# Performance work log

Hardware: AMD Instinct MI355X
Metric: run time of the kernel (lower is better)

The kernel has to match this reference:

```python
import jax, jax.numpy as jnp
import numpy as np

WS = 7
SHIFT = 3
NH = 16
DIM = 512
MLP = 2048
EMB = 512
EPS = 1e-6


def _rel_pos_index(ws):
    coords = np.stack(np.meshgrid(np.arange(ws), np.arange(ws), indexing='ij'))  # [2,ws,ws]
    flat = coords.reshape(2, -1)
    rel = flat[:, :, None] - flat[:, None, :]          # [2,N,N]
    rel = rel.transpose(1, 2, 0).copy()                # [N,N,2]
    rel[..., 0] += ws - 1
    rel[..., 1] += ws - 1
    rel[..., 0] *= 2 * ws - 1
    return rel.sum(-1)                                 # [N,N] int


def _shift_mask(H, W, ws, shift):
    img = np.zeros((H, W))
    cnt = 0
    for hs in (slice(0, -ws), slice(-ws, -shift), slice(-shift, None)):
        for wsl in (slice(0, -ws), slice(-ws, -shift), slice(-shift, None)):
            img[hs, wsl] = cnt
            cnt += 1
    win = img.reshape(H // ws, ws, W // ws, ws).transpose(0, 2, 1, 3).reshape(-1, ws * ws)
    diff = win[:, None, :] - win[:, :, None]           # [nW,N,N]
    return np.where(diff != 0, -100.0, 0.0).astype(np.float32)


def setup_inputs() -> dict:
    key = jax.random.key(0)
    ks = jax.random.split(key, 16)
    B, H, W = 16, 56, 56
    C, mlp, emb_dim = DIM, MLP, EMB
    std = 0.02
    inp = {
        'x': jax.random.normal(ks[0], (B, H * W, C), jnp.float32),
        'emb': jax.random.normal(ks[1], (B, emb_dim), jnp.float32),
        'adaLN_w': jax.random.normal(ks[2], (emb_dim, 6 * C), jnp.float32) * std,
        'adaLN_b': jnp.zeros((6 * C,), jnp.float32),
        'qkv_w': jax.random.normal(ks[3], (C, 3 * C), jnp.float32) * std,
        'qkv_b': jnp.zeros((3 * C,), jnp.float32),
        'proj_w': jax.random.normal(ks[4], (C, C), jnp.float32) * std,
        'proj_b': jnp.zeros((C,), jnp.float32),
        'rel_bias_table': jax.random.normal(ks[5], ((2 * WS - 1) ** 2, NH), jnp.float32) * std,
        'ff_w1': jax.random.normal(ks[6], (C, mlp), jnp.float32) * std,
        'ff_b1': jnp.zeros((mlp,), jnp.float32),
        'ff_w2': jax.random.normal(ks[7], (mlp, C), jnp.float32) * std,
        'ff_b2': jnp.zeros((C,), jnp.float32),
        'H': H,
        'W': W,
    }
    return inp


def _ln(t):
    mu = t.mean(-1, keepdims=True)
    var = ((t - mu) ** 2).mean(-1, keepdims=True)
    return (t - mu) / jnp.sqrt(var + EPS)


def reference(x, emb, adaLN_w, adaLN_b, qkv_w, qkv_b, proj_w, proj_b,
              rel_bias_table, ff_w1, ff_b1, ff_w2, ff_b2, H, W):
    B, L, C = x.shape
    dh = C // NH
    scale = dh ** (-0.5)
    N = WS * WS
    nWh, nWw = H // WS, W // WS
    nW = nWh * nWw

    # AdaLN modulation
    mod = jax.nn.silu(emb) @ adaLN_w + adaLN_b
    sh_sa, sc_sa, g_sa, sh_ff, sc_ff, g_ff = jnp.split(mod, 6, axis=-1)

    h = _ln(x) * (1.0 + sc_sa[:, None, :]) + sh_sa[:, None, :]
    h = h.reshape(B, H, W, C)
    h = jnp.roll(h, (-SHIFT, -SHIFT), axis=(1, 2))

    # window partition -> [B*nW, N, C]
    win = h.reshape(B, nWh, WS, nWw, WS, C).transpose(0, 1, 3, 2, 4, 5).reshape(B * nW, N, C)

    qkv = (win @ qkv_w + qkv_b).reshape(B * nW, N, 3, NH, dh).transpose(2, 0, 3, 1, 4)
    q, k, v = qkv[0], qkv[1], qkv[2]                   # [B_, NH, N, dh]
    attn = jnp.einsum('bhnd,bhmd->bhnm', q, k) * scale

    idx = _rel_pos_index(WS)
    bias = rel_bias_table[idx.reshape(-1)].reshape(N, N, NH).transpose(2, 0, 1)
    attn = attn + bias[None]

    mask = jnp.asarray(_shift_mask(H, W, WS, SHIFT))   # [nW,N,N]
    attn = attn.reshape(B, nW, NH, N, N) + mask[None, :, None]
    attn = jax.nn.softmax(attn.reshape(B * nW, NH, N, N), axis=-1)

    out = jnp.einsum('bhnm,bhmd->bnhd', attn, v).reshape(B * nW, N, C)
    out = out @ proj_w + proj_b

    # window reverse + unshift
    h = out.reshape(B, nWh, nWw, WS, WS, C).transpose(0, 1, 3, 2, 4, 5).reshape(B, H, W, C)
    h = jnp.roll(h, (SHIFT, SHIFT), axis=(1, 2)).reshape(B, L, C)

    x = x + g_sa[:, None, :] * h

    h = _ln(x) * (1.0 + sc_ff[:, None, :]) + sh_ff[:, None, :]
    ffo = jax.nn.gelu(h @ ff_w1 + ff_b1, approximate=False) @ ff_w2 + ff_b2
    return x + g_ff[:, None, :] * ffo
```

## Files before the change

kernel.cpp:

```cpp
#include <hip/hip_runtime.h>
#include <cmath>

typedef unsigned short u16;
typedef unsigned short u16x2 __attribute__((ext_vector_type(2)));
typedef unsigned short u16x4 __attribute__((ext_vector_type(4)));
typedef unsigned short u16x8 __attribute__((ext_vector_type(8)));
typedef short s16x8 __attribute__((ext_vector_type(8)));
typedef float f32x4 __attribute__((ext_vector_type(4)));
typedef float f32x2 __attribute__((ext_vector_type(2)));

#define B_SZ 16
#define HW 56
#define L_TOK 3136
#define C_DIM 512
#define NHEAD 16
#define DHEAD 32
#define WS7 7
#define NWIN 49
#define ROWS_TOTAL 50176
#define MLP_DIM 2048

__device__ __forceinline__ float bf2f(u16 u) {
    union { unsigned int i; float f; } z;
    z.i = ((unsigned int)u) << 16;
    return z.f;
}
__device__ __forceinline__ u16 f2bf(float f) {
    union { float f; unsigned int i; } z;
    z.f = f;
    unsigned int r = z.i + 0x7fffu + ((z.i >> 16) & 1u);
    return (u16)(r >> 16);
}

__device__ __forceinline__ void gl_lds16(const u16* g, u16* l) {
    __builtin_amdgcn_global_load_lds(
        (const __attribute__((address_space(1))) unsigned int*)g,
        (__attribute__((address_space(3))) unsigned int*)l,
        16, 0, 0);
}

__global__ __launch_bounds__(256)
void mod_kernel(const float* __restrict__ emb, const float* __restrict__ w,
                const float* __restrict__ bias, float* __restrict__ mod)
{
    int b = blockIdx.y;
    int o = blockIdx.x * 256 + threadIdx.x;
    __shared__ float se[512];
    for (int i = threadIdx.x; i < 512; i += 256) {
        float e = emb[b * 512 + i];
        se[i] = e / (1.0f + expf(-e));
    }
    __syncthreads();
    float acc = bias[o];
    #pragma unroll 8
    for (int k = 0; k < 512; ++k)
        acc += se[k] * w[(size_t)k * 3072 + o];
    mod[b * 3072 + o] = acc;
}

__global__ __launch_bounds__(1024)
void transpose_kernel(const float* __restrict__ W, u16* __restrict__ Wt, int K, int N)
{
    __shared__ float tile[32][33];
    int k0 = blockIdx.x * 32, n0 = blockIdx.y * 32;
    tile[threadIdx.y][threadIdx.x] = W[(size_t)(k0 + threadIdx.y) * N + (n0 + threadIdx.x)];
    __syncthreads();
    Wt[(size_t)(n0 + threadIdx.y) * K + (k0 + threadIdx.x)] = f2bf(tile[threadIdx.x][threadIdx.y]);
}

template<int WINDOWED>
__global__ __launch_bounds__(256)
void ln_kernel(const float* __restrict__ xin, const float* __restrict__ mod,
               u16* __restrict__ out, int shOff, int scOff, int rowBase)
{
    int wv   = threadIdx.x >> 6;
    int lane = threadIdx.x & 63;
    int rbl = blockIdx.x * 4 + wv;
    int rb  = rbl + rowBase;
    int b = rb / L_TOK, l = rb - b * L_TOK;
    const float* xr = xin + (size_t)rb * C_DIM;
    int c0 = lane * 8;
    f32x4 u0 = *(const f32x4*)(xr + c0);
    f32x4 u1 = *(const f32x4*)(xr + c0 + 4);
    float s = u0.x + u0.y + u0.z + u0.w + u1.x + u1.y + u1.z + u1.w;
    float q = u0.x*u0.x + u0.y*u0.y + u0.z*u0.z + u0.w*u0.w
            + u1.x*u1.x + u1.y*u1.y + u1.z*u1.z + u1.w*u1.w;
    #pragma unroll
    for (int off = 32; off > 0; off >>= 1) {
        s += __shfl_xor(s, off);
        q += __shfl_xor(q, off);
    }
    float mu = s * (1.0f / 512.0f);
    float var = q * (1.0f / 512.0f) - mu * mu;
    float rstd = rsqrtf(var + 1e-6f);
    const float* mb = mod + b * 3072;
    f32x4 sc0 = *(const f32x4*)(mb + scOff + c0);
    f32x4 sc1 = *(const f32x4*)(mb + scOff + c0 + 4);
    f32x4 sh0 = *(const f32x4*)(mb + shOff + c0);
    f32x4 sh1 = *(const f32x4*)(mb + shOff + c0 + 4);
    float y[8];
    y[0] = (u0.x - mu) * rstd * (1.0f + sc0.x) + sh0.x;
    y[1] = (u0.y - mu) * rstd * (1.0f + sc0.y) + sh0.y;
    y[2] = (u0.z - mu) * rstd * (1.0f + sc0.z) + sh0.z;
    y[3] = (u0.w - mu) * rstd * (1.0f + sc0.w) + sh0.w;
    y[4] = (u1.x - mu) * rstd * (1.0f + sc1.x) + sh1.x;
    y[5] = (u1.y - mu) * rstd * (1.0f + sc1.y) + sh1.y;
    y[6] = (u1.z - mu) * rstd * (1.0f + sc1.z) + sh1.z;
    y[7] = (u1.w - mu) * rstd * (1.0f + sc1.w) + sh1.w;
    size_t drow;
    if (WINDOWED) {
        int hh = l / HW, ww = l - hh * HW;
        int hs = hh - 3; if (hs < 0) hs += HW;
        int ws2 = ww - 3; if (ws2 < 0) ws2 += HW;
        int wi = (hs / WS7) * 8 + (ws2 / WS7);
        int n  = (hs % WS7) * WS7 + (ws2 % WS7);
        int b_local = rbl / L_TOK;
        drow = (size_t)((b_local * 64 + wi) * NWIN + n);
    } else {
        drow = (size_t)rbl;
    }
    u16x8 o;
    #pragma unroll
    for (int i = 0; i < 8; ++i) o[i] = f2bf(y[i]);
    *(u16x8*)(out + drow * C_DIM + c0) = o;
}

template<int EPI>
__global__ __launch_bounds__(512, 2)
void gemm256(const u16* __restrict__ A, const u16* __restrict__ Bt,
             const float* __restrict__ bias, void* __restrict__ outv,
             const float* __restrict__ resid, const float* __restrict__ mod,
             int N, int K, int rowOffset, int nyb)
{
    __shared__ u16 sA[4][256][32];
    __shared__ u16 sB[4][256][32];
    const int tid  = threadIdx.x;
    const int lane = tid & 63;
    const int wave = tid >> 6;
    const int wm = wave >> 1;
    const int wn = wave & 1;
    const int quad = lane >> 4;
    const int mrow = lane & 15;

    const int nwg  = gridDim.x;
    const int orig = blockIdx.x;
    const int xq = nwg >> 3, xr = nwg & 7;
    const int xcd = orig & 7, xidx = orig >> 3;
    const int wgid = (xcd < xr ? xcd * (xq + 1)
                               : xr * (xq + 1) + (xcd - xr) * xq) + xidx;
    const int bx = wgid / nyb;
    const int by = wgid - bx * nyb;
    const int rowBase = bx * 256;
    const int colBase = by * 256;

    const int r0   = wave * 32;
    const int lrow = lane >> 2;
    const int lcol = ((lane & 3) ^ ((lane >> 3) & 3)) * 8;
    const u16* gA = A  + (size_t)(rowBase + r0 + lrow) * K + lcol;
    const u16* gB = Bt + (size_t)(colBase + r0 + lrow) * K + lcol;
    const size_t gstep = (size_t)16 * K;
    const int cq = (quad ^ ((mrow >> 1) & 3)) * 8;

    f32x4 acc[4][8] = {};
    const int nt = K >> 5;

#define STAGE(bi, kk) do {                                 \
    gl_lds16(gA + (kk),         &sA[bi][r0][0]);           \
    gl_lds16(gA + (kk) + gstep, &sA[bi][r0 + 16][0]);      \
    gl_lds16(gB + (kk),         &sB[bi][r0][0]);           \
    gl_lds16(gB + (kk) + gstep, &sB[bi][r0 + 16][0]);      \
} while (0)

#define COMPUTE(bi)                                                        \
    {                                                                      \
        s16x8 af[4], bg[8];                                                \
        _Pragma("unroll")                                                  \
        for (int tt = 0; tt < 4; ++tt)                                     \
            af[tt] = *(const s16x8*)&sA[bi][wm * 64 + tt * 16 + mrow][cq]; \
        _Pragma("unroll")                                                  \
        for (int tn = 0; tn < 8; ++tn)                                     \
            bg[tn] = *(const s16x8*)&sB[bi][wn * 128 + tn * 16 + mrow][cq];\
        _Pragma("unroll")                                                  \
        for (int tm = 0; tm < 4; ++tm)                                     \
            _Pragma("unroll")                                              \
            for (int tn = 0; tn < 8; ++tn)                                 \
                acc[tm][tn] = __builtin_amdgcn_mfma_f32_16x16x32_bf16(     \
                    af[tm], bg[tn], acc[tm][tn], 0, 0, 0);                 \
    }

#define WAIT8() asm volatile("s_waitcnt vmcnt(8) lgkmcnt(0)" ::: "memory")
#define WAIT4() asm volatile("s_waitcnt vmcnt(4) lgkmcnt(0)" ::: "memory")
#define WAIT0() asm volatile("s_waitcnt vmcnt(0) lgkmcnt(0)" ::: "memory")
#define BAR()   do { __builtin_amdgcn_s_barrier();                         \
                     __builtin_amdgcn_sched_barrier(0); } while (0)

    STAGE(0, 0);
    STAGE(1, 32);
    STAGE(2, 64);

    for (int t = 0; t < nt - 4; t += 4) {
        WAIT8(); BAR(); STAGE(3, (t + 3) << 5); COMPUTE(0);
        WAIT8(); BAR(); STAGE(0, (t + 4) << 5); COMPUTE(1);
        WAIT8(); BAR(); STAGE(1, (t + 5) << 5); COMPUTE(2);
        WAIT8(); BAR(); STAGE(2, (t + 6) << 5); COMPUTE(3);
    }
    WAIT8(); BAR(); STAGE(3, (nt - 1) << 5); COMPUTE(0);
    WAIT8(); BAR(); COMPUTE(1);
    WAIT4(); BAR(); COMPUTE(2);
    WAIT0(); BAR(); COMPUTE(3);

#undef STAGE
#undef COMPUTE
#undef WAIT8
#undef WAIT4
#undef WAIT0
#undef BAR

    #pragma unroll
    for (int tm = 0; tm < 4; ++tm) {
        #pragma unroll
        for (int tn = 0; tn < 8; ++tn) {
            int col = colBase + wn * 128 + tn * 16 + mrow;
            float bv = bias[col];
            #pragma unroll
            for (int i = 0; i < 4; ++i) {
                int r = rowBase + wm * 64 + tm * 16 + quad * 4 + i;
                float v = acc[tm][tn][i] + bv;
                if constexpr (EPI == 0) {
                    ((u16*)outv)[(size_t)r * N + col] = f2bf(v);
                } else if constexpr (EPI == 1) {
                    float g = 0.5f * v * (1.0f + erff(v * 0.70710678118654752f));
                    ((u16*)outv)[(size_t)r * N + col] = f2bf(g);
                } else if constexpr (EPI == 2) {
                    int rg = r + rowOffset;
                    int b = rg / L_TOK;
                    int rem = rg - b * L_TOK;
                    int wi = rem / NWIN;
                    int n  = rem - wi * NWIN;
                    int hs  = (wi >> 3) * WS7 + n / WS7;
                    int ws2 = (wi & 7) * WS7 + n % WS7;
                    int hh = hs + 3;  if (hh >= HW)  hh -= HW;
                    int ww = ws2 + 3; if (ww >= HW)  ww -= HW;
                    size_t dst = ((size_t)(b * L_TOK + hh * HW + ww)) * C_DIM + col;
                    float g = mod[b * 3072 + 1024 + col];
                    ((float*)outv)[dst] = resid[dst] + g * v;
                } else {
                    int rg = r + rowOffset;
                    int b = rg / L_TOK;
                    size_t dst = (size_t)rg * C_DIM + col;
                    float g = mod[b * 3072 + 2560 + col];
                    ((float*)outv)[dst] = resid[dst] + g * v;
                }
            }
        }
    }
}

__global__ __launch_bounds__(256)
void attn_mfma(const u16* __restrict__ qkv, const float* __restrict__ bias_table,
               u16* __restrict__ out)
{
    const int w    = blockIdx.x;
    const int hg   = blockIdx.y;
    const int wave = threadIdx.x >> 6;
    const int lane = threadIdx.x & 63;
    const int h    = hg * 4 + wave;
    const int wi   = w & 63;
    const int quad = lane >> 4;
    const int mrow = lane & 15;

    __shared__ u16 sP[4][64][72];
    __shared__ u16 sVt[4][32][72];
    __shared__ float sBias[4][169];

    const u16* qb = qkv + (size_t)w * NWIN * 1536 + h * DHEAD;

    for (int e = lane; e < 169; e += 64)
        sBias[wave][e] = bias_table[e * NHEAD + h];

    #pragma unroll
    for (int rr = 0; rr < 4; ++rr) {
        int e = rr * 64 + lane;
        int r = e >> 2, d0 = (e & 3) * 8;
        u16x8 vv = {};
        if (e < 196)
            vv = *(const u16x8*)(qb + (size_t)r * 1536 + 1024 + d0);
        #pragma unroll
        for (int j = 0; j < 8; ++j)
            sVt[wave][d0 + j][r] = vv[j];
    }

    s16x8 qf[4], kf[4];
    #pragma unroll
    for (int t = 0; t < 4; ++t) {
        int r = t * 16 + mrow; if (r > 48) r = 48;
        qf[t] = *(const s16x8*)(qb + (size_t)r * 1536 + quad * 8);
        kf[t] = *(const s16x8*)(qb + (size_t)r * 1536 + 512 + quad * 8);
    }
    __syncthreads();

    f32x4 sacc[4][4] = {};
    #pragma unroll
    for (int tm = 0; tm < 4; ++tm)
        #pragma unroll
        for (int tn = 0; tn < 4; ++tn)
            sacc[tm][tn] = __builtin_amdgcn_mfma_f32_16x16x32_bf16(
                qf[tm], kf[tn], sacc[tm][tn], 0, 0, 0);

    const float scale = 0.17677669529663687f;
    const int wh = wi >> 3, ww = wi & 7;

    int khA[4], kwA[4], rkA[4], nOK[4];
    #pragma unroll
    for (int tn = 0; tn < 4; ++tn) {
        int n = tn * 16 + mrow;
        nOK[tn] = (n < NWIN);
        int nc = n > 48 ? 48 : n;
        khA[tn] = nc / 7; kwA[tn] = nc - khA[tn] * 7;
        int gkh = wh * 7 + khA[tn], gkw = ww * 7 + kwA[tn];
        rkA[tn] = (gkh < 49 ? 0 : (gkh < 53 ? 1 : 2)) * 3
                + (gkw < 49 ? 0 : (gkw < 53 ? 1 : 2));
    }

    #pragma unroll
    for (int tm = 0; tm < 4; ++tm) {
        #pragma unroll
        for (int i = 0; i < 4; ++i) {
            int m = tm * 16 + quad * 4 + i;
            int mc = m > 48 ? 48 : m;
            int qh = mc / 7, qw = mc - qh * 7;
            int gqh = wh * 7 + qh, gqw = ww * 7 + qw;
            int rq = (gqh < 49 ? 0 : (gqh < 53 ? 1 : 2)) * 3
                   + (gqw < 49 ? 0 : (gqw < 53 ? 1 : 2));
            float v[4];
            #pragma unroll
            for (int tn = 0; tn < 4; ++tn) {
                float s = sacc[tm][tn][i] * scale;
                s += sBias[wave][(qh - khA[tn] + 6) * 13 + (qw - kwA[tn] + 6)];
                if (rq != rkA[tn]) s -= 100.0f;
                v[tn] = nOK[tn] ? s : -1e30f;
            }
            float mx = fmaxf(fmaxf(v[0], v[1]), fmaxf(v[2], v[3]));
            mx = fmaxf(mx, __shfl_xor(mx, 1));
            mx = fmaxf(mx, __shfl_xor(mx, 2));
            mx = fmaxf(mx, __shfl_xor(mx, 4));
            mx = fmaxf(mx, __shfl_xor(mx, 8));
            float p0 = __expf(v[0] - mx), p1 = __expf(v[1] - mx);
            float p2 = __expf(v[2] - mx), p3 = __expf(v[3] - mx);
            float sum = p0 + p1 + p2 + p3;
            sum += __shfl_xor(sum, 1);
            sum += __shfl_xor(sum, 2);
            sum += __shfl_xor(sum, 4);
            sum += __shfl_xor(sum, 8);
            float inv = 1.0f / sum;
            float pp[4] = { p0 * inv, p1 * inv, p2 * inv, p3 * inv };
            #pragma unroll
            for (int tn = 0; tn < 4; ++tn) {
                float po = __shfl_xor(pp[tn], 1);
                if (!(mrow & 1)) {
                    unsigned int pk = (unsigned int)f2bf(pp[tn])
                                    | ((unsigned int)f2bf(po) << 16);
                    *(unsigned int*)&sP[wave][m][tn * 16 + mrow] = pk;
                }
            }
        }
    }
    __syncthreads();

    f32x4 oacc[2][4] = {};
    #pragma unroll
    for (int ks = 0; ks < 2; ++ks) {
        s16x8 vf[2], pf[4];
        #pragma unroll
        for (int td = 0; td < 2; ++td)
            vf[td] = *(const s16x8*)&sVt[wave][td * 16 + mrow][ks * 32 + quad * 8];
        #pragma unroll
        for (int tm = 0; tm < 4; ++tm)
            pf[tm] = *(const s16x8*)&sP[wave][tm * 16 + mrow][ks * 32 + quad * 8];
        #pragma unroll
        for (int td = 0; td < 2; ++td)
            #pragma unroll
            for (int tm = 0; tm < 4; ++tm)
                oacc[td][tm] = __builtin_amdgcn_mfma_f32_16x16x32_bf16(
                    vf[td], pf[tm], oacc[td][tm], 0, 0, 0);
    }

    #pragma unroll
    for (int tm = 0; tm < 4; ++tm) {
        int m = tm * 16 + mrow;
        if (m < NWIN) {
            u16* orow = out + ((size_t)(w * NWIN + m)) * C_DIM + h * DHEAD;
            #pragma unroll
            for (int td = 0; td < 2; ++td) {
                u16x4 ov;
                #pragma unroll
                for (int i = 0; i < 4; ++i) ov[i] = f2bf(oacc[td][tm][i]);
                *(u16x4*)(orow + td * 16 + quad * 4) = ov;
            }
        }
    }
}

extern "C" void kernel_launch(void* const* d_in, const int* in_sizes, int n_in,
                              void* d_out, int out_size, void* d_ws, size_t ws_size,
                              hipStream_t stream)
{
    const float* x       = (const float*)d_in[0];
    const float* emb     = (const float*)d_in[1];
    const float* adaLN_w = (const float*)d_in[2];
    const float* adaLN_b = (const float*)d_in[3];
    const float* qkv_w   = (const float*)d_in[4];
    const float* qkv_b   = (const float*)d_in[5];
    const float* proj_w  = (const float*)d_in[6];
    const float* proj_b  = (const float*)d_in[7];
    const float* relb    = (const float*)d_in[8];
    const float* ff_w1   = (const float*)d_in[9];
    const float* ff_b1   = (const float*)d_in[10];
    const float* ff_w2   = (const float*)d_in[11];
    const float* ff_b2   = (const float*)d_in[12];
    float* outp = (float*)d_out;

    char* ws = (char*)d_ws;
    float* mod   = (float*)(ws + 0);
    u16* wT_qkv  = (u16*)(ws + 196608);
    u16* wT_proj = (u16*)(ws + 1769472);
    u16* wT_ff1  = (u16*)(ws + 2293760);
    u16* wT_ff2  = (u16*)(ws + 4390912);
    char* slots  = ws + 6488064;

    const size_t perB_S = (size_t)L_TOK * C_DIM * sizeof(u16);
    const size_t perB_L = (size_t)L_TOK * MLP_DIM * sizeof(u16);

    int CB = 4;
    if (ws_size >= 6488064 + 8  * (perB_S + perB_L)) CB = 8;
    if (ws_size >= 6488064 + 16 * (perB_S + perB_L)) CB = 16;

    const int nChunks   = B_SZ / CB;
    const int chunkRows = CB * L_TOK;
    const int nrb       = chunkRows / 256;
    u16* slotS = (u16*)slots;
    u16* slotL = (u16*)(slots + (size_t)CB * perB_S);

    mod_kernel<<<dim3(12, 16), dim3(256), 0, stream>>>(emb, adaLN_w, adaLN_b, mod);
    transpose_kernel<<<dim3(16, 48), dim3(32, 32), 0, stream>>>(qkv_w,  wT_qkv, 512, 1536);
    transpose_kernel<<<dim3(16, 16), dim3(32, 32), 0, stream>>>(proj_w, wT_proj, 512, 512);
    transpose_kernel<<<dim3(16, 64), dim3(32, 32), 0, stream>>>(ff_w1,  wT_ff1, 512, 2048);
    transpose_kernel<<<dim3(64, 16), dim3(32, 32), 0, stream>>>(ff_w2,  wT_ff2, 2048, 512);

    for (int c = 0; c < nChunks; ++c) {
        int row0 = c * chunkRows;
        ln_kernel<1><<<dim3(chunkRows / 4), dim3(256), 0, stream>>>(
            x, mod, slotS, 0, 512, row0);
        gemm256<0><<<dim3(nrb * 6), dim3(512), 0, stream>>>(
            slotS, wT_qkv, qkv_b, slotL, nullptr, mod, 1536, 512, 0, 6);
        attn_mfma<<<dim3(CB * 64, 4), dim3(256), 0, stream>>>(slotL, relb, slotS);
        gemm256<2><<<dim3(nrb * 2), dim3(512), 0, stream>>>(
            slotS, wT_proj, proj_b, outp, x, mod, 512, 512, row0, 2);
        ln_kernel<0><<<dim3(chunkRows / 4), dim3(256), 0, stream>>>(
            outp, mod, slotS, 1536, 2048, row0);
        gemm256<1><<<dim3(nrb * 8), dim3(512), 0, stream>>>(
            slotS, wT_ff1, ff_b1, slotL, nullptr, mod, 2048, 512, 0, 8);
        gemm256<3><<<dim3(nrb * 2), dim3(512), 0, stream>>>(
            slotL, wT_ff2, ff_b2, outp, outp, mod, 512, 2048, row0, 2);
    }
}
```

Measured before the change: 1.013 ms.

## Restructure GEMM main loop into phased ping-pong schedule with 2x4 wave layout

The 256x256 bf16 GEMM changes its wave layout from 4x2 to 2x4. Each wave now owns a 128x64 sub-tile. The K loop moves from four 32-wide stages to 64-wide double-buffered tiles, split into four phases per tile. Each phase interleaves fine-grained global-to-LDS loads with an MFMA cluster bracketed by barriers and s_setprio, to overlap memory traffic with matrix math and cut LDS reads per MFMA. The launch_bounds occupancy hint of 2 is dropped, and the extra barriers per phase add sync overhead.

```diff
diff --git a/kernel.cpp b/kernel.cpp
--- a/kernel.cpp
+++ b/kernel.cpp
@@ -126,19 +126,19 @@
 }
 
 template<int EPI>
-__global__ __launch_bounds__(512, 2)
+__global__ __launch_bounds__(512)
 void gemm256(const u16* __restrict__ A, const u16* __restrict__ Bt,
              const float* __restrict__ bias, void* __restrict__ outv,
              const float* __restrict__ resid, const float* __restrict__ mod,
              int N, int K, int rowOffset, int nyb)
 {
-    __shared__ u16 sA[4][256][32];
-    __shared__ u16 sB[4][256][32];
+    __shared__ u16 sA[2][2][256][32];
+    __shared__ u16 sB[2][2][256][32];
     const int tid  = threadIdx.x;
     const int lane = tid & 63;
     const int wave = tid >> 6;
-    const int wm = wave >> 1;
-    const int wn = wave & 1;
+    const int wm = wave >> 2;
+    const int wn = wave & 3;
     const int quad = lane >> 4;
     const int mrow = lane & 15;
 
@@ -153,79 +153,89 @@
     const int rowBase = bx * 256;
     const int colBase = by * 256;
 
-    const int r0   = wave * 32;
-    const int lrow = lane >> 2;
-    const int lcol = ((lane & 3) ^ ((lane >> 3) & 3)) * 8;
-    const u16* gA = A  + (size_t)(rowBase + r0 + lrow) * K + lcol;
-    const u16* gB = Bt + (size_t)(colBase + r0 + lrow) * K + lcol;
-    const size_t gstep = (size_t)16 * K;
-    const int cq = (quad ^ ((mrow >> 1) & 3)) * 8;
-
-    f32x4 acc[4][8] = {};
-    const int nt = K >> 5;
-
-#define STAGE(bi, kk) do {                                 \
-    gl_lds16(gA + (kk),         &sA[bi][r0][0]);           \
-    gl_lds16(gA + (kk) + gstep, &sA[bi][r0 + 16][0]);      \
-    gl_lds16(gB + (kk),         &sB[bi][r0][0]);           \
-    gl_lds16(gB + (kk) + gstep, &sB[bi][r0 + 16][0]);      \
+    const int laneRow = lane >> 2;
+    const int swz = ((lane & 3) ^ ((lane >> 3) & 3)) * 8;
+    const u16* pA0 = A  + (size_t)(rowBase + wave * 32 + laneRow) * K + swz;
+    const u16* pA1 = pA0 + (size_t)16 * K;
+    const u16* pB0 = Bt + (size_t)(colBase + wave * 32 + laneRow) * K + swz;
+    const u16* pB1 = pB0 + (size_t)16 * K;
+    const int cq8 = (quad ^ ((mrow >> 1) & 3)) * 8;
+
+    f32x4 acc[8][4] = {};
+    s16x8 af[4], bg[4];
+    const int NKT  = K >> 6;
+    const int nkt4 = NKT << 2;
+
+#define STAGE_E(idx) do {                                            \
+    const int _kt = (idx) >> 2, _e = (idx) & 3;                      \
+    const int _buf = _kt & 1, _kh = _e >> 1;                         \
+    const int _ko = _kt * 64 + _kh * 32;                             \
+    if (_e & 1) {                                                    \
+        gl_lds16(pB0 + _ko, &sB[_buf][_kh][wave * 32][0]);           \
+        gl_lds16(pB1 + _ko, &sB[_buf][_kh][wave * 32 + 16][0]);      \
+    } else {                                                         \
+        gl_lds16(pA0 + _ko, &sA[_buf][_kh][wave * 32][0]);           \
+        gl_lds16(pA1 + _ko, &sA[_buf][_kh][wave * 32 + 16][0]);      \
+    }                                                                \
 } while (0)
 
-#define COMPUTE(bi)                                                        \
-    {                                                                      \
-        s16x8 af[4], bg[8];                                                \
-        _Pragma("unroll")                                                  \
-        for (int tt = 0; tt < 4; ++tt)                                     \
-            af[tt] = *(const s16x8*)&sA[bi][wm * 64 + tt * 16 + mrow][cq]; \
-        _Pragma("unroll")                                                  \
-        for (int tn = 0; tn < 8; ++tn)                                     \
-            bg[tn] = *(const s16x8*)&sB[bi][wn * 128 + tn * 16 + mrow][cq];\
-        _Pragma("unroll")                                                  \
-        for (int tm = 0; tm < 4; ++tm)                                     \
-            _Pragma("unroll")                                              \
-            for (int tn = 0; tn < 8; ++tn)                                 \
-                acc[tm][tn] = __builtin_amdgcn_mfma_f32_16x16x32_bf16(     \
-                    af[tm], bg[tn], acc[tm][tn], 0, 0, 0);                 \
-    }
-
-#define WAIT8() asm volatile("s_waitcnt vmcnt(8) lgkmcnt(0)" ::: "memory")
-#define WAIT4() asm volatile("s_waitcnt vmcnt(4) lgkmcnt(0)" ::: "memory")
-#define WAIT0() asm volatile("s_waitcnt vmcnt(0) lgkmcnt(0)" ::: "memory")
-#define BAR()   do { __builtin_amdgcn_s_barrier();                         \
-                     __builtin_amdgcn_sched_barrier(0); } while (0)
-
-    STAGE(0, 0);
-    STAGE(1, 32);
-    STAGE(2, 64);
-
-    for (int t = 0; t < nt - 4; t += 4) {
-        WAIT8(); BAR(); STAGE(3, (t + 3) << 5); COMPUTE(0);
-        WAIT8(); BAR(); STAGE(0, (t + 4) << 5); COMPUTE(1);
-        WAIT8(); BAR(); STAGE(1, (t + 5) << 5); COMPUTE(2);
-        WAIT8(); BAR(); STAGE(2, (t + 6) << 5); COMPUTE(3);
-    }
-    WAIT8(); BAR(); STAGE(3, (nt - 1) << 5); COMPUTE(0);
-    WAIT8(); BAR(); COMPUTE(1);
-    WAIT4(); BAR(); COMPUTE(2);
-    WAIT0(); BAR(); COMPUTE(3);
-
-#undef STAGE
-#undef COMPUTE
-#undef WAIT8
-#undef WAIT4
-#undef WAIT0
-#undef BAR
-
-    #pragma unroll
-    for (int tm = 0; tm < 4; ++tm) {
-        #pragma unroll
-        for (int tn = 0; tn < 8; ++tn) {
-            int col = colBase + wn * 128 + tn * 16 + mrow;
+#define PHASE(_mh, _ks, _rdB) do {                                           \
+    _Pragma("unroll")                                                        \
+    for (int mi = 0; mi < 4; ++mi)                                           \
+        af[mi] = *(const s16x8*)                                             \
+            &sA[buf][_ks][wm * 128 + ((_mh) * 4 + mi) * 16 + mrow][cq8];     \
+    if (_rdB) {                                                              \
+        _Pragma("unroll")                                                    \
+        for (int nf = 0; nf < 4; ++nf)                                       \
+            bg[nf] = *(const s16x8*)                                         \
+                &sB[buf][_ks][wn * 64 + nf * 16 + mrow][cq8];                \
+    }                                                                        \
+    if (sidx < nkt4) STAGE_E(sidx);                                          \
+    ++sidx;                                                                  \
+    __builtin_amdgcn_s_barrier();                                            \
+    asm volatile("s_waitcnt lgkmcnt(0)" ::: "memory");                       \
+    __builtin_amdgcn_sched_barrier(0);                                       \
+    __builtin_amdgcn_s_setprio(1);                                           \
+    _Pragma("unroll")                                                        \
+    for (int mi = 0; mi < 4; ++mi)                                           \
+        _Pragma("unroll")                                                    \
+        for (int nf = 0; nf < 4; ++nf)                                       \
+            acc[(_mh) * 4 + mi][nf] = __builtin_amdgcn_mfma_f32_16x16x32_bf16( \
+                af[mi], bg[nf], acc[(_mh) * 4 + mi][nf], 0, 0, 0);           \
+    __builtin_amdgcn_s_setprio(0);                                           \
+    __builtin_amdgcn_s_barrier();                                            \
+    __builtin_amdgcn_sched_barrier(0);                                       \
+} while (0)
+
+    int sidx = 6;
+    STAGE_E(0); STAGE_E(1); STAGE_E(2); STAGE_E(3); STAGE_E(4); STAGE_E(5);
+
+    for (int kt = 0; kt < NKT; ++kt) {
+        const int buf = kt & 1;
+        if (kt == NKT - 1)
+            asm volatile("s_waitcnt vmcnt(0)" ::: "memory");
+        else
+            asm volatile("s_waitcnt vmcnt(4)" ::: "memory");
+        __builtin_amdgcn_s_barrier();
+        __builtin_amdgcn_sched_barrier(0);
+        PHASE(0, 0, true);
+        PHASE(1, 0, false);
+        PHASE(0, 1, true);
+        PHASE(1, 1, false);
+    }
+#undef STAGE_E
+#undef PHASE
+
+    #pragma unroll
+    for (int mf = 0; mf < 8; ++mf) {
+        #pragma unroll
+        for (int nf = 0; nf < 4; ++nf) {
+            int col = colBase + wn * 64 + nf * 16 + mrow;
             float bv = bias[col];
             #pragma unroll
             for (int i = 0; i < 4; ++i) {
-                int r = rowBase + wm * 64 + tm * 16 + quad * 4 + i;
-                float v = acc[tm][tn][i] + bv;
+                int r = rowBase + wm * 128 + mf * 16 + quad * 4 + i;
+                float v = acc[mf][nf][i] + bv;
                 if constexpr (EPI == 0) {
                     ((u16*)outv)[(size_t)r * N + col] = f2bf(v);
                 } else if constexpr (EPI == 1) {
```

New measurement: 985.4 us. 1.03x faster.
